# Optimization experiments

Measured on AMD Instinct MI355X. Metric: run time of the kernel, lower is better.

## Reference

```python
import jax, jax.numpy as jnp
import numpy as np

B, S1, S2 = 8, 2048, 2048
K1_DIM = K2_DIM = 512
PK1_DIM = PK2_DIM = 256
ATT_DIM = 512
DV = 512


def setup_inputs() -> dict:
    key = jax.random.key(0)
    ks = jax.random.split(key, 16)
    s = 0.02
    inp = {
        "k1": jax.random.normal(ks[0], (B, S1, K1_DIM), jnp.float32),
        "k2": jax.random.normal(ks[1], (B, S2, K2_DIM), jnp.float32),
        "preserved_k1": jax.random.normal(ks[2], (B, S1, PK1_DIM), jnp.float32),
        "preserved_k2": jax.random.normal(ks[3], (B, S2, PK2_DIM), jnp.float32),
        "v1": jax.random.normal(ks[4], (B, S1, DV), jnp.float32),
        "v2": jax.random.normal(ks[5], (B, S2, DV), jnp.float32),
        # Linear params stored as [in, out] (x @ W + b == torch Linear)
        "W_k1": jax.random.normal(ks[6], (K1_DIM, ATT_DIM), jnp.float32) * s,
        "b_k1": jnp.zeros((ATT_DIM,), jnp.float32),
        "W_k2": jax.random.normal(ks[7], (K2_DIM, ATT_DIM), jnp.float32) * s,
        "b_k2": jnp.zeros((ATT_DIM,), jnp.float32),
        "W_pk1": jax.random.normal(ks[8], (K1_DIM + PK1_DIM, ATT_DIM), jnp.float32) * s,
        "b_pk1": jnp.zeros((ATT_DIM,), jnp.float32),
        "W_pk2": jax.random.normal(ks[9], (K2_DIM + PK2_DIM, ATT_DIM), jnp.float32) * s,
        "b_pk2": jnp.zeros((ATT_DIM,), jnp.float32),
        # lengths in [S/2, S) so no softmax row is fully masked (original exits on NaN)
        "k1_lengths": jax.random.randint(ks[10], (B,), S1 // 2, S1, jnp.int32).astype(jnp.int64),
        "k2_lengths": jax.random.randint(ks[11], (B,), S2 // 2, S2, jnp.int32).astype(jnp.int64),
    }
    return inp


def _mask(k1_lengths, k2_lengths):
    # Faithful to the original loop: a position is masked iff EXACTLY ONE of
    # (row >= l1) / (col >= l2) holds (mask counter == 1, not >= 1).
    row_over = (jnp.arange(S1)[None, :, None] >= k1_lengths[:, None, None])  # [B,S1,1]
    col_over = (jnp.arange(S2)[None, None, :] >= k2_lengths[:, None, None])  # [B,1,S2]
    return (row_over.astype(jnp.int32) + col_over.astype(jnp.int32)) == 1  # [B,S1,S2]


def reference(k1, k2, preserved_k1, preserved_k2, v1, v2,
              W_k1, b_k1, W_k2, b_k2, W_pk1, b_pk1, W_pk2, b_pk2,
              k1_lengths, k2_lengths):
    pk1 = jnp.concatenate([k1, preserved_k1], axis=-1) @ W_pk1 + b_pk1  # [B,S1,A]
    pk2 = jnp.concatenate([k2, preserved_k2], axis=-1) @ W_pk2 + b_pk2  # [B,S2,A]
    k1p = k1 @ W_k1 + b_k1  # [B,S1,A]
    k2p = k2 @ W_k2 + b_k2  # [B,S2,A]

    score_1 = jnp.einsum("bsa,bta->bst", k1p, pk2)   # [B,S1,S2]
    score_2 = jnp.einsum("bsa,bta->bst", pk1, k2p)   # [B,S1,S2]

    mask = _mask(k1_lengths, k2_lengths)
    score_1 = jnp.where(mask, -jnp.inf, score_1)
    score_2 = jnp.where(mask, -jnp.inf, score_2)

    w1 = jax.nn.softmax(jnp.swapaxes(score_1, 1, 2), axis=-1)  # [B,S2,S1]
    w2 = jax.nn.softmax(score_2, axis=-1)                      # [B,S1,S2]

    o1 = jnp.einsum("bts,bsd->btd", w1, v1)  # [B,S2,DV]
    o2 = jnp.einsum("bst,btd->bsd", w2, v2)  # [B,S1,DV]
    # NOTE: original returns ragged per-sample slices of w1/w2; we return the
    # full padded weight matrices (slice w1[i,:l2,:l1], w2[i,:l1,:l2] to match).
    return (o1, o2, w1, w2)
```

## Files before the change

### kernel.cpp

```cpp
#include <hip/hip_runtime.h>

typedef _Float16 half8 __attribute__((ext_vector_type(8)));
typedef float    floatx4 __attribute__((ext_vector_type(4)));
typedef unsigned short u16;

constexpr int Bn  = 8;
constexpr int Sq  = 2048;
constexpr int KD  = 512;
constexpr int PKD = 256;
constexpr int AD  = 512;
constexpr int DV  = 512;

__device__ __forceinline__ void llds16(const void* g, void* l)
{
    __builtin_amdgcn_global_load_lds(
        (const __attribute__((address_space(1))) unsigned int*)g,
        (__attribute__((address_space(3))) unsigned int*)l, 16, 0, 0);
}

__global__ __launch_bounds__(256)
void transpose_cast_k(const float* __restrict__ in, _Float16* __restrict__ out,
                      int inRows, int inCols, long long bsIn, long long bsOut)
{
    __shared__ float t[32][33];
    const int b = blockIdx.z;
    in  += (long long)b * bsIn;
    out += (long long)b * bsOut;
    const int tx = threadIdx.x & 31;
    const int ty = threadIdx.x >> 5;
    const int c0 = blockIdx.x * 32;
    const int r0 = blockIdx.y * 32;
#pragma unroll
    for (int i = 0; i < 4; ++i)
        t[ty + 8*i][tx] = in[(long long)(r0 + ty + 8*i) * inCols + c0 + tx];
    __syncthreads();
#pragma unroll
    for (int i = 0; i < 4; ++i)
        out[(long long)(c0 + ty + 8*i) * inRows + r0 + tx] = (_Float16)t[tx][ty + 8*i];
}

__global__ __launch_bounds__(256)
void cast_cat_k(const float* __restrict__ x, const float* __restrict__ y,
                _Float16* __restrict__ out)
{
    const int idx = blockIdx.x * 256 + threadIdx.x;
    const int e   = idx * 8;
    const int r   = e / 768;
    const int c   = e % 768;
    const float* src = (c < 512) ? (x + (long long)r * 512 + c)
                                 : (y + (long long)r * 256 + (c - 512));
    const floatx4 f0 = *(const floatx4*)(src);
    const floatx4 f1 = *(const floatx4*)(src + 4);
    half8 h;
#pragma unroll
    for (int j = 0; j < 4; ++j) { h[j] = (_Float16)f0[j]; h[4 + j] = (_Float16)f1[j]; }
    *(half8*)(out + (long long)e) = h;
}

template<bool A_F32, bool OUT_F16>
__global__ __launch_bounds__(256, 2)
void gemm_k(const void* __restrict__ A1v, const void* __restrict__ A2v, int Ksplit,
            int lda1, int lda2, long long bsA,
            const _Float16* __restrict__ Bm, int ldb, long long bsB,
            void* __restrict__ Cv, int ldc, long long bsC,
            const float* __restrict__ bias, int K)
{
    __shared__ __align__(16) unsigned char AsRaw[A_F32 ? 16384 : 8192];
    __shared__ __align__(16) unsigned char BsRaw[8192];

    const int tid  = threadIdx.x;
    const int lane = tid & 63;
    const int wave = tid >> 6;
    const int wm   = (wave >> 1) * 64;
    const int wn   = (wave & 1) * 64;
    const int fr   = lane & 15;
    const int fq   = lane >> 4;

    const int tm = blockIdx.y, tn = blockIdx.x, bz = blockIdx.z;
    const long long aRowBase = (long long)tm * 128;
    const long long bRowBase = (long long)tn * 128;
    const _Float16* Bbase = Bm + (long long)bz * bsB;

    floatx4 acc[4][4];
#pragma unroll
    for (int i = 0; i < 4; ++i)
#pragma unroll
        for (int j = 0; j < 4; ++j) acc[i][j] = (floatx4)0.0f;

    for (int k0 = 0; k0 < K; k0 += 32) {
        __syncthreads();

        if (A_F32) {
            const float* A1 = (const float*)A1v + (long long)bz * bsA;
            const float* A2 = (const float*)A2v;
#pragma unroll
            for (int is = 0; is < 4; ++is) {
                const int r  = (tid >> 3) + is * 32;
                const int ch = (tid & 7) ^ (r & 7);
                const int kk = k0 + ch * 4;
                const float* src = (kk < Ksplit)
                    ? A1 + (aRowBase + r) * lda1 + kk
                    : A2 + (aRowBase + r) * lda2 + (kk - Ksplit);
                llds16(src, AsRaw + tid * 16 + is * 4096);
            }
        } else {
            const _Float16* A1 = (const _Float16*)A1v + (long long)bz * bsA;
#pragma unroll
            for (int is = 0; is < 2; ++is) {
                const int r  = (tid >> 2) + is * 64;
                const int ch = (tid & 3) ^ (r & 3);
                llds16(A1 + (aRowBase + r) * lda1 + k0 + ch * 8,
                       AsRaw + tid * 16 + is * 4096);
            }
        }
#pragma unroll
        for (int is = 0; is < 2; ++is) {
            const int r  = (tid >> 2) + is * 64;
            const int ch = (tid & 3) ^ (r & 3);
            llds16(Bbase + (bRowBase + r) * ldb + k0 + ch * 8,
                   BsRaw + tid * 16 + is * 4096);
        }

        __syncthreads();

        half8 af[4], bf[4];
        if (A_F32) {
            const float* As32 = (const float*)AsRaw;
#pragma unroll
            for (int i = 0; i < 4; ++i) {
                const int r  = wm + i * 16 + fr;
                const int c0 = ((2 * fq) ^ (r & 7)) * 4;
                const int c1 = ((2 * fq + 1) ^ (r & 7)) * 4;
                floatx4 f0 = *(const floatx4*)(As32 + r * 32 + c0);
                floatx4 f1 = *(const floatx4*)(As32 + r * 32 + c1);
                half8 h;
#pragma unroll
                for (int j = 0; j < 4; ++j) {
                    h[j]     = (_Float16)f0[j];
                    h[4 + j] = (_Float16)f1[j];
                }
                af[i] = h;
            }
        } else {
            const _Float16* As16 = (const _Float16*)AsRaw;
#pragma unroll
            for (int i = 0; i < 4; ++i) {
                const int r  = wm + i * 16 + fr;
                const int ch = fq ^ (r & 3);
                af[i] = *(const half8*)(As16 + r * 32 + ch * 8);
            }
        }
        {
            const _Float16* Bs16 = (const _Float16*)BsRaw;
#pragma unroll
            for (int j = 0; j < 4; ++j) {
                const int r  = wn + j * 16 + fr;
                const int ch = fq ^ (r & 3);
                bf[j] = *(const half8*)(Bs16 + r * 32 + ch * 8);
            }
        }
#pragma unroll
        for (int i = 0; i < 4; ++i)
#pragma unroll
            for (int j = 0; j < 4; ++j)
                acc[i][j] = __builtin_amdgcn_mfma_f32_16x16x32_f16(af[i], bf[j], acc[i][j], 0, 0, 0);
    }

    const int crow0 = tm * 128 + wm + fq * 4;
    const int ccol0 = tn * 128 + wn + fr;
    if (OUT_F16) {
        _Float16* C = (_Float16*)Cv + (long long)bz * bsC;
#pragma unroll
        for (int i = 0; i < 4; ++i)
#pragma unroll
            for (int j = 0; j < 4; ++j) {
                const int col = ccol0 + j * 16;
                const float bv = bias[col];
#pragma unroll
                for (int r = 0; r < 4; ++r)
                    C[(long long)(crow0 + i*16 + r) * ldc + col] = (_Float16)(acc[i][j][r] + bv);
            }
    } else {
        float* C = (float*)Cv + (long long)bz * bsC;
#pragma unroll
        for (int i = 0; i < 4; ++i)
#pragma unroll
            for (int j = 0; j < 4; ++j) {
                const int col = ccol0 + j * 16;
#pragma unroll
                for (int r = 0; r < 4; ++r)
                    C[(long long)(crow0 + i*16 + r) * ldc + col] = acc[i][j][r];
            }
    }
}

__global__ __launch_bounds__(512, 2)
void gemm256_k(const _Float16* __restrict__ Am, long long bsA, int lda,
               const _Float16* __restrict__ Bm, long long bsB, int ldb,
               float* __restrict__ Cm, long long bsC, int ldc, int K)
{
    __shared__ __align__(16) _Float16 lds[65536];

    const int lin0 = (blockIdx.z * 8 + blockIdx.y) * 8 + blockIdx.x;
    const int lin  = (lin0 & 7) * 64 + (lin0 >> 3);
    const int tn   = lin & 7;
    const int tm   = (lin >> 3) & 7;
    const int bz   = lin >> 6;

    const int tid  = threadIdx.x;
    const int lane = tid & 63;
    const int wave = tid >> 6;
    const int wm   = (wave >> 2) * 128;
    const int wn   = (wave & 3) * 64;
    const int fr   = lane & 15;
    const int fq   = lane >> 4;

    const _Float16* Ab = Am + (long long)bz * bsA + (long long)tm * 256 * lda;
    const _Float16* Bb = Bm + (long long)bz * bsB + (long long)tn * 256 * ldb;

    const int sr = lane >> 3;
    const int ch = (lane & 7) ^ sr;
    const _Float16* srcA[2][2];
    const _Float16* srcB[2][2];
#pragma unroll
    for (int h = 0; h < 2; ++h)
#pragma unroll
        for (int l = 0; l < 2; ++l) {
            const int r = h * 128 + (wave * 2 + l) * 8 + sr;
            srcA[h][l] = Ab + (long long)r * lda + ch * 8;
            srcB[h][l] = Bb + (long long)r * ldb + ch * 8;
        }

    auto stageA = [&](int kt, int buf) {
#pragma unroll
        for (int h = 0; h < 2; ++h)
#pragma unroll
            for (int l = 0; l < 2; ++l)
                llds16(srcA[h][l] + kt * 64,
                       lds + buf * 32768 + h * 8192 + (wave * 2 + l) * 512 + lane * 8);
    };
    auto stageB = [&](int kt, int buf) {
#pragma unroll
        for (int h = 0; h < 2; ++h)
#pragma unroll
            for (int l = 0; l < 2; ++l)
                llds16(srcB[h][l] + kt * 64,
                       lds + buf * 32768 + 16384 + h * 8192 + (wave * 2 + l) * 512 + lane * 8);
    };

    auto rdA = [&](int buf, int im, int kk) -> half8 {
        const int row = wm + im * 16 + fr;
        const int c   = (kk * 4 + fq) ^ (row & 7);
        return *(const half8*)(lds + buf * 32768 + row * 64 + c * 8);
    };
    auto rdB = [&](int buf, int jn, int kk) -> half8 {
        const int row = wn + jn * 16 + fr;
        const int c   = (kk * 4 + fq) ^ (row & 7);
        return *(const half8*)(lds + buf * 32768 + 16384 + row * 64 + c * 8);
    };

    floatx4 acc[8][4];
#pragma unroll
    for (int i = 0; i < 8; ++i)
#pragma unroll
        for (int j = 0; j < 4; ++j) acc[i][j] = (floatx4)0.0f;

    const int KT = K >> 6;

    stageA(0, 0);
    stageB(0, 0);
    __syncthreads();

    for (int kt = 0; kt < KT; ++kt) {
        const int buf = kt & 1;
        half8 af[4][2], bf[2][2];
#pragma unroll
        for (int q = 0; q < 4; ++q) {
            const int nh = q >> 1;
            const int mh = (q == 1 || q == 2) ? 1 : 0;
            if (q == 0 || q == 2) {
#pragma unroll
                for (int j = 0; j < 2; ++j)
#pragma unroll
                    for (int kk = 0; kk < 2; ++kk)
                        bf[j][kk] = rdB(buf, nh * 2 + j, kk);
            }
            if (q != 2) {
#pragma unroll
                for (int i = 0; i < 4; ++i)
#pragma unroll
                    for (int kk = 0; kk < 2; ++kk)
                        af[i][kk] = rdA(buf, mh * 4 + i, kk);
            }
            if (kt + 1 < KT) {
                if (q == 0)      stageA(kt + 1, buf ^ 1);
                else if (q == 1) stageB(kt + 1, buf ^ 1);
            }
            __builtin_amdgcn_s_barrier();
            __builtin_amdgcn_s_setprio(1);
#pragma unroll
            for (int i = 0; i < 4; ++i)
#pragma unroll
                for (int j = 0; j < 2; ++j)
#pragma unroll
                    for (int kk = 0; kk < 2; ++kk)
                        acc[mh * 4 + i][nh * 2 + j] =
                            __builtin_amdgcn_mfma_f32_16x16x32_f16(
                                af[i][kk], bf[j][kk], acc[mh * 4 + i][nh * 2 + j], 0, 0, 0);
            __builtin_amdgcn_s_setprio(0);
            if (q < 3) __builtin_amdgcn_s_barrier();
        }
        __syncthreads();
    }

    float* Cb = Cm + (long long)bz * bsC;
    const int crow0 = tm * 256 + wm + fq * 4;
    const int ccol0 = tn * 256 + wn + fr;
#pragma unroll
    for (int i = 0; i < 8; ++i)
#pragma unroll
        for (int j = 0; j < 4; ++j) {
            const long long base = (long long)(crow0 + i * 16) * ldc + ccol0 + j * 16;
#pragma unroll
            for (int r = 0; r < 4; ++r)
                Cb[base + (long long)r * ldc] = acc[i][j][r];
        }
}

template<bool OUT_F16>
__global__ __launch_bounds__(512, 2)
void gemm256x128_k(const _Float16* __restrict__ A0, const _Float16* __restrict__ A1,
                   long long bsA, int lda,
                   const _Float16* __restrict__ B0, const _Float16* __restrict__ B1,
                   long long bsB, int ldb,
                   void* __restrict__ C0, void* __restrict__ C1,
                   long long bsC, int ldc,
                   const float* __restrict__ bias0, const float* __restrict__ bias1,
                   int K, int zsplit)
{
    __shared__ __align__(16) _Float16 lds[49152];

    const int gx   = gridDim.x, gy = gridDim.y;
    const int nwg  = gx * gy * gridDim.z;
    const int lin0 = (blockIdx.z * gy + blockIdx.y) * gx + blockIdx.x;
    const int cpx  = nwg >> 3;
    const int lin  = (lin0 & 7) * cpx + (lin0 >> 3);
    const int tn   = lin % gx;
    const int tmp2 = lin / gx;
    const int tm   = tmp2 % gy;
    const int bz   = tmp2 / gy;

    const bool sel = (bz >= zsplit);
    const int  bzl = sel ? (bz - zsplit) : bz;
    const _Float16* Am = sel ? A1 : A0;
    const _Float16* Bm = sel ? B1 : B0;

    const int tid  = threadIdx.x;
    const int lane = tid & 63;
    const int wave = tid >> 6;
    const int wm   = (wave >> 2) * 128;
    const int wn   = (wave & 3) * 32;
    const int fr   = lane & 15;
    const int fq   = lane >> 4;

    const _Float16* Ab = Am + (long long)bzl * bsA + (long long)tm * 256 * lda;
    const _Float16* Bb = Bm + (long long)bzl * bsB + (long long)tn * 128 * ldb;

    const int sr = lane >> 3;
    const int ch = (lane & 7) ^ sr;
    const _Float16* srcA[2][2];
    const _Float16* srcB[2];
#pragma unroll
    for (int h = 0; h < 2; ++h)
#pragma unroll
        for (int l = 0; l < 2; ++l)
            srcA[h][l] = Ab + (long long)(h * 128 + (wave * 2 + l) * 8 + sr) * lda + ch * 8;
#pragma unroll
    for (int l = 0; l < 2; ++l)
        srcB[l] = Bb + (long long)((wave * 2 + l) * 8 + sr) * ldb + ch * 8;

    auto stageA = [&](int kt, int buf) {
#pragma unroll
        for (int h = 0; h < 2; ++h)
#pragma unroll
            for (int l = 0; l < 2; ++l)
                llds16(srcA[h][l] + kt * 64,
                       lds + buf * 24576 + h * 8192 + (wave * 2 + l) * 512 + lane * 8);
    };
    auto stageB = [&](int kt, int buf) {
#pragma unroll
        for (int l = 0; l < 2; ++l)
            llds16(srcB[l] + kt * 64,
                   lds + buf * 24576 + 16384 + (wave * 2 + l) * 512 + lane * 8);
    };

    auto rdA = [&](int buf, int im, int kk) -> half8 {
        const int row = wm + im * 16 + fr;
        const int c   = (kk * 4 + fq) ^ (row & 7);
        return *(const half8*)(lds + buf * 24576 + row * 64 + c * 8);
    };
    auto rdB = [&](int buf, int jn, int kk) -> half8 {
        const int row = wn + jn * 16 + fr;
        const int c   = (kk * 4 + fq) ^ (row & 7);
        return *(const half8*)(lds + buf * 24576 + 16384 + row * 64 + c * 8);
    };

    floatx4 acc[8][2];
#pragma unroll
    for (int i = 0; i < 8; ++i)
#pragma unroll
        for (int j = 0; j < 2; ++j) acc[i][j] = (floatx4)0.0f;

    const int KT = K >> 6;

    stageA(0, 0);
    stageB(0, 0);
    __syncthreads();

    for (int kt = 0; kt < KT; ++kt) {
        const int buf = kt & 1;
        half8 afA[4][2], afB[4][2], bf0[2], bf1[2];

#pragma unroll
        for (int kk = 0; kk < 2; ++kk) bf0[kk] = rdB(buf, 0, kk);
#pragma unroll
        for (int i = 0; i < 4; ++i)
#pragma unroll
            for (int kk = 0; kk < 2; ++kk) afA[i][kk] = rdA(buf, i, kk);
        if (kt + 1 < KT) stageA(kt + 1, buf ^ 1);
        __builtin_amdgcn_s_barrier();
        __builtin_amdgcn_s_setprio(1);
#pragma unroll
        for (int i = 0; i < 4; ++i)
#pragma unroll
            for (int kk = 0; kk < 2; ++kk)
                acc[i][0] = __builtin_amdgcn_mfma_f32_16x16x32_f16(afA[i][kk], bf0[kk], acc[i][0], 0, 0, 0);
        __builtin_amdgcn_s_setprio(0);
        __builtin_amdgcn_s_barrier();

#pragma unroll
        for (int i = 0; i < 4; ++i)
#pragma unroll
            for (int kk = 0; kk < 2; ++kk) afB[i][kk] = rdA(buf, 4 + i, kk);
        if (kt + 1 < KT) stageB(kt + 1, buf ^ 1);
        __builtin_amdgcn_s_barrier();
        __builtin_amdgcn_s_setprio(1);
#pragma unroll
        for (int i = 0; i < 4; ++i)
#pragma unroll
            for (int kk = 0; kk < 2; ++kk)
                acc[4 + i][0] = __builtin_amdgcn_mfma_f32_16x16x32_f16(afB[i][kk], bf0[kk], acc[4 + i][0], 0, 0, 0);
        __builtin_amdgcn_s_setprio(0);
        __builtin_amdgcn_s_barrier();

#pragma unroll
        for (int kk = 0; kk < 2; ++kk) bf1[kk] = rdB(buf, 1, kk);
        __builtin_amdgcn_s_barrier();
        __builtin_amdgcn_s_setprio(1);
#pragma unroll
        for (int i = 0; i < 4; ++i)
#pragma unroll
            for (int kk = 0; kk < 2; ++kk)
                acc[4 + i][1] = __builtin_amdgcn_mfma_f32_16x16x32_f16(afB[i][kk], bf1[kk], acc[4 + i][1], 0, 0, 0);
        __builtin_amdgcn_s_setprio(0);
        __builtin_amdgcn_s_barrier();

        __builtin_amdgcn_s_setprio(1);
#pragma unroll
        for (int i = 0; i < 4; ++i)
#pragma unroll
            for (int kk = 0; kk < 2; ++kk)
                acc[i][1] = __builtin_amdgcn_mfma_f32_16x16x32_f16(afA[i][kk], bf1[kk], acc[i][1], 0, 0, 0);
        __builtin_amdgcn_s_setprio(0);

        __syncthreads();
    }

    const int crow0 = tm * 256 + wm + fq * 4;
    const int ccol0 = tn * 128 + wn + fr;
    if (OUT_F16) {
        const float* bias = sel ? bias1 : bias0;
        _Float16* C = (_Float16*)(sel ? C1 : C0) + (long long)bzl * bsC;
#pragma unroll
        for (int i = 0; i < 8; ++i)
#pragma unroll
            for (int j = 0; j < 2; ++j) {
                const int col = ccol0 + j * 16;
                const float bv = bias[col];
#pragma unroll
                for (int r = 0; r < 4; ++r)
                    C[(long long)(crow0 + i * 16 + r) * ldc + col] = (_Float16)(acc[i][j][r] + bv);
            }
    } else {
        float* C = (float*)(sel ? C1 : C0) + (long long)bzl * bsC;
#pragma unroll
        for (int i = 0; i < 8; ++i)
#pragma unroll
            for (int j = 0; j < 2; ++j) {
                const int col = ccol0 + j * 16;
#pragma unroll
                for (int r = 0; r < 4; ++r)
                    C[(long long)(crow0 + i * 16 + r) * ldc + col] = acc[i][j][r];
            }
    }
}

__device__ __forceinline__ int load_len(const int* __restrict__ p, int b)
{
    return (p[1] == 0) ? p[2 * b] : p[b];
}

__global__ __launch_bounds__(256)
void softmax_mask_k(float* __restrict__ w, _Float16* __restrict__ wh,
                    const int* __restrict__ lenR, const int* __restrict__ lenC)
{
    const int b = blockIdx.y;
    const int r = blockIdx.x;
    const long long rowOff = ((long long)b * Sq + r) * (long long)Sq;
    float* row = w + rowOff;
    const int lr = load_len(lenR, b);
    const int lc = load_len(lenC, b);
    const bool rover = (r >= lr);
    const int tid  = threadIdx.x;
    const int lane = tid & 63;
    const int wave = tid >> 6;

    floatx4 x0 = *(const floatx4*)(row + tid * 8);
    floatx4 x1 = *(const floatx4*)(row + tid * 8 + 4);
    float v[8];
#pragma unroll
    for (int j = 0; j < 4; ++j) { v[j] = x0[j]; v[4 + j] = x1[j]; }

    float m = -3.0e38f;
#pragma unroll
    for (int j = 0; j < 8; ++j) {
        const int c = tid * 8 + j;
        if (rover != (c >= lc)) v[j] = -__builtin_inff();
        m = fmaxf(m, v[j]);
    }
#pragma unroll
    for (int off = 32; off > 0; off >>= 1) m = fmaxf(m, __shfl_xor(m, off, 64));
    __shared__ float redm[4], reds[4];
    if (lane == 0) redm[wave] = m;
    __syncthreads();
    m = fmaxf(fmaxf(redm[0], redm[1]), fmaxf(redm[2], redm[3]));

    float s = 0.f;
#pragma unroll
    for (int j = 0; j < 8; ++j) { v[j] = __expf(v[j] - m); s += v[j]; }
#pragma unroll
    for (int off = 32; off > 0; off >>= 1) s += __shfl_xor(s, off, 64);
    if (lane == 0) reds[wave] = s;
    __syncthreads();
    s = reds[0] + reds[1] + reds[2] + reds[3];
    const float inv = 1.0f / s;
#pragma unroll
    for (int j = 0; j < 4; ++j) { x0[j] = v[j] * inv; x1[j] = v[4 + j] * inv; }
    *(floatx4*)(row + tid * 8)     = x0;
    *(floatx4*)(row + tid * 8 + 4) = x1;
    if (wh != nullptr) {
        half8 h;
#pragma unroll
        for (int j = 0; j < 4; ++j) { h[j] = (_Float16)x0[j]; h[4 + j] = (_Float16)x1[j]; }
        *(half8*)(wh + rowOff + tid * 8) = h;
    }
}

extern "C" void kernel_launch(void* const* d_in, const int* in_sizes, int n_in,
                              void* d_out, int out_size, void* d_ws, size_t ws_size,
                              hipStream_t stream)
{
    (void)in_sizes; (void)n_in; (void)out_size;
    const float* k1    = (const float*)d_in[0];
    const float* k2    = (const float*)d_in[1];
    const float* pk1in = (const float*)d_in[2];
    const float* pk2in = (const float*)d_in[3];
    const float* v1    = (const float*)d_in[4];
    const float* v2    = (const float*)d_in[5];
    const float* W_k1  = (const float*)d_in[6];
    const float* b_k1  = (const float*)d_in[7];
    const float* W_k2  = (const float*)d_in[8];
    const float* b_k2  = (const float*)d_in[9];
    const float* W_pk1 = (const float*)d_in[10];
    const float* b_pk1 = (const float*)d_in[11];
    const float* W_pk2 = (const float*)d_in[12];
    const float* b_pk2 = (const float*)d_in[13];
    const int* len1 = (const int*)d_in[14];
    const int* len2 = (const int*)d_in[15];

    float* out = (float*)d_out;
    float* o1 = out;
    float* o2 = o1 + (long long)Bn * Sq * DV;
    float* w1 = o2 + (long long)Bn * Sq * DV;
    float* w2 = w1 + (long long)Bn * Sq * Sq;

    _Float16* k1p = (_Float16*)o1;
    _Float16* k2p = k1p + (long long)Bn * Sq * AD;
    _Float16* pk1 = (_Float16*)o2;
    _Float16* pk2 = pk1 + (long long)Bn * Sq * AD;
    _Float16* cat1 = pk2 + (long long)Bn * Sq * AD;
    _Float16* cat2 = cat1 + (long long)Bn * Sq * (KD + PKD);

    _Float16* vT1   = (_Float16*)d_ws;
    _Float16* vT2   = vT1 + (long long)Bn * DV * Sq;
    _Float16* WTk1  = vT2 + (long long)Bn * DV * Sq;
    _Float16* WTk2  = WTk1 + AD * KD;
    _Float16* WTpk1 = WTk2 + AD * KD;
    _Float16* WTpk2 = WTpk1 + AD * (KD + PKD);

    const unsigned long long fixedHalves =
        2ull * Bn * DV * Sq + 2ull * AD * KD + 2ull * AD * (KD + PKD);
    _Float16* w1h = (_Float16*)d_ws + fixedHalves;
    _Float16* w2h = w1h + (long long)Bn * Sq * Sq;
    const bool fast =
        ws_size >= (fixedHalves + 2ull * Bn * Sq * Sq) * sizeof(_Float16);

    transpose_cast_k<<<dim3(AD/32, KD/32, 1), 256, 0, stream>>>(W_k1, WTk1, KD, AD, 0, 0);
    transpose_cast_k<<<dim3(AD/32, KD/32, 1), 256, 0, stream>>>(W_k2, WTk2, KD, AD, 0, 0);
    transpose_cast_k<<<dim3(AD/32, (KD+PKD)/32, 1), 256, 0, stream>>>(W_pk1, WTpk1, KD+PKD, AD, 0, 0);
    transpose_cast_k<<<dim3(AD/32, (KD+PKD)/32, 1), 256, 0, stream>>>(W_pk2, WTpk2, KD+PKD, AD, 0, 0);
    transpose_cast_k<<<dim3(DV/32, Sq/32, Bn), 256, 0, stream>>>(v1, vT1, Sq, DV,
        (long long)Sq*DV, (long long)Sq*DV);
    transpose_cast_k<<<dim3(DV/32, Sq/32, Bn), 256, 0, stream>>>(v2, vT2, Sq, DV,
        (long long)Sq*DV, (long long)Sq*DV);
    cast_cat_k<<<dim3((Bn*Sq*(KD+PKD))/(256*8), 1, 1), 256, 0, stream>>>(k1, pk1in, cat1);
    cast_cat_k<<<dim3((Bn*Sq*(KD+PKD))/(256*8), 1, 1), 256, 0, stream>>>(k2, pk2in, cat2);

    gemm256x128_k<true><<<dim3(AD/128, (Bn*Sq)/256, 2), 512, 0, stream>>>(
        cat1, cat2, 0, KD+PKD,
        WTk1, WTk2, 0, KD,
        k1p, k2p, 0, AD,
        b_k1, b_k2, KD, 1);
    gemm256x128_k<true><<<dim3(AD/128, (Bn*Sq)/256, 2), 512, 0, stream>>>(
        cat1, cat2, 0, KD+PKD,
        WTpk1, WTpk2, 0, KD+PKD,
        pk1, pk2, 0, AD,
        b_pk1, b_pk2, KD+PKD, 1);

    const dim3 gScore(Sq/256, Sq/256, Bn);
    gemm256_k<<<gScore, 512, 0, stream>>>(
        pk2, (long long)Sq*AD, AD,
        k1p, (long long)Sq*AD, AD,
        w1, (long long)Sq*Sq, Sq, AD);
    gemm256_k<<<gScore, 512, 0, stream>>>(
        pk1, (long long)Sq*AD, AD,
        k2p, (long long)Sq*AD, AD,
        w2, (long long)Sq*Sq, Sq, AD);

    softmax_mask_k<<<dim3(Sq, Bn), 256, 0, stream>>>(w1, fast ? w1h : nullptr, len2, len1);
    softmax_mask_k<<<dim3(Sq, Bn), 256, 0, stream>>>(w2, fast ? w2h : nullptr, len1, len2);

    if (fast) {
        gemm256x128_k<false><<<dim3(DV/128, Sq/256, 2*Bn), 512, 0, stream>>>(
            w1h, w2h, (long long)Sq*Sq, Sq,
            vT1, vT2, (long long)DV*Sq, Sq,
            o1, o2, (long long)Sq*DV, DV,
            nullptr, nullptr, Sq, Bn);
    } else {
        const dim3 gOut(DV/128, Sq/128, Bn);
        gemm_k<true, false><<<gOut, 256, 0, stream>>>(
            w1, w1, Sq, Sq, Sq, (long long)Sq*Sq,
            vT1, Sq, (long long)DV*Sq,
            o1, DV, (long long)Sq*DV, nullptr, Sq);
        gemm_k<true, false><<<gOut, 256, 0, stream>>>(
            w2, w2, Sq, Sq, Sq, (long long)Sq*Sq,
            vT2, Sq, (long long)DV*Sq,
            o2, DV, (long long)Sq*DV, nullptr, Sq);
    }
}
```

Baseline: 854.1 us.

## Merge launches and write score matrices as fp16 before softmax

```diff
diff --git a/kernel.cpp b/kernel.cpp
--- a/kernel.cpp
+++ b/kernel.cpp
@@ -19,13 +19,17 @@
 }
 
 __global__ __launch_bounds__(256)
-void transpose_cast_k(const float* __restrict__ in, _Float16* __restrict__ out,
-                      int inRows, int inCols, long long bsIn, long long bsOut)
+void transpose_cast_k(const float* __restrict__ in0, const float* __restrict__ in1,
+                      _Float16* __restrict__ out0, _Float16* __restrict__ out1,
+                      int inRows, int inCols, long long bsIn, long long bsOut,
+                      int zsplit)
 {
     __shared__ float t[32][33];
-    const int b = blockIdx.z;
-    in  += (long long)b * bsIn;
-    out += (long long)b * bsOut;
+    const int bz = blockIdx.z;
+    const bool sel = (bz >= zsplit);
+    const int b = sel ? bz - zsplit : bz;
+    const float* in = (sel ? in1 : in0) + (long long)b * bsIn;
+    _Float16* out = (sel ? out1 : out0) + (long long)b * bsOut;
     const int tx = threadIdx.x & 31;
     const int ty = threadIdx.x >> 5;
     const int c0 = blockIdx.x * 32;
@@ -40,9 +44,42 @@
 }
 
 __global__ __launch_bounds__(256)
-void cast_cat_k(const float* __restrict__ x, const float* __restrict__ y,
-                _Float16* __restrict__ out)
-{
+void wT_all_k(const float* __restrict__ Wk1, const float* __restrict__ Wk2,
+              const float* __restrict__ Wpk1, const float* __restrict__ Wpk2,
+              _Float16* __restrict__ Tk1, _Float16* __restrict__ Tk2,
+              _Float16* __restrict__ Tpk1, _Float16* __restrict__ Tpk2)
+{
+    const int z = blockIdx.z;
+    const float* W; _Float16* T; int Krows;
+    if      (z == 0) { W = Wk1;  T = Tk1;  Krows = KD; }
+    else if (z == 1) { W = Wk2;  T = Tk2;  Krows = KD; }
+    else if (z == 2) { W = Wpk1; T = Tpk1; Krows = KD + PKD; }
+    else             { W = Wpk2; T = Tpk2; Krows = KD + PKD; }
+    const int r0 = blockIdx.y * 32;
+    if (r0 >= Krows) return;
+    const int c0 = blockIdx.x * 32;
+    __shared__ float t[32][33];
+    const int tx = threadIdx.x & 31;
+    const int ty = threadIdx.x >> 5;
+#pragma unroll
+    for (int i = 0; i < 4; ++i)
+        t[ty + 8*i][tx] = W[(long long)(r0 + ty + 8*i) * AD + c0 + tx];
+    __syncthreads();
+#pragma unroll
+    for (int i = 0; i < 4; ++i)
+        T[(long long)(c0 + ty + 8*i) * Krows + r0 + tx] = (_Float16)t[tx][ty + 8*i];
+}
+
+__global__ __launch_bounds__(256)
+void cast_cat_k(const float* __restrict__ x0, const float* __restrict__ y0,
+                _Float16* __restrict__ o0,
+                const float* __restrict__ x1, const float* __restrict__ y1,
+                _Float16* __restrict__ o1)
+{
+    const bool sel = (blockIdx.z != 0);
+    const float* x = sel ? x1 : x0;
+    const float* y = sel ? y1 : y0;
+    _Float16* out = sel ? o1 : o0;
     const int idx = blockIdx.x * 256 + threadIdx.x;
     const int e   = idx * 8;
     const int r   = e / 768;
@@ -194,18 +231,28 @@
     }
 }
 
+template<bool OUT16>
 __global__ __launch_bounds__(512, 2)
-void gemm256_k(const _Float16* __restrict__ Am, long long bsA, int lda,
-               const _Float16* __restrict__ Bm, long long bsB, int ldb,
-               float* __restrict__ Cm, long long bsC, int ldc, int K)
+void gemm256_k(const _Float16* __restrict__ A0, const _Float16* __restrict__ A1,
+               const _Float16* __restrict__ B0, const _Float16* __restrict__ B1,
+               void* __restrict__ C0v, void* __restrict__ C1v,
+               long long bsA, int lda, long long bsB, int ldb,
+               long long bsC, int ldc, int K, int zsplit)
 {
     __shared__ __align__(16) _Float16 lds[65536];
 
+    const int nwg  = 64 * gridDim.z;
     const int lin0 = (blockIdx.z * 8 + blockIdx.y) * 8 + blockIdx.x;
-    const int lin  = (lin0 & 7) * 64 + (lin0 >> 3);
+    const int cpx  = nwg >> 3;
+    const int lin  = (lin0 & 7) * cpx + (lin0 >> 3);
     const int tn   = lin & 7;
     const int tm   = (lin >> 3) & 7;
     const int bz   = lin >> 6;
+
+    const bool sel = (bz >= zsplit);
+    const int  bzl = sel ? (bz - zsplit) : bz;
+    const _Float16* Am = sel ? A1 : A0;
+    const _Float16* Bm = sel ? B1 : B0;
 
     const int tid  = threadIdx.x;
     const int lane = tid & 63;
@@ -215,8 +262,8 @@
     const int fr   = lane & 15;
     const int fq   = lane >> 4;
 
-    const _Float16* Ab = Am + (long long)bz * bsA + (long long)tm * 256 * lda;
-    const _Float16* Bb = Bm + (long long)bz * bsB + (long long)tn * 256 * ldb;
+    const _Float16* Ab = Am + (long long)bzl * bsA + (long long)tm * 256 * lda;
+    const _Float16* Bb = Bm + (long long)bzl * bsB + (long long)tn * 256 * ldb;
 
     const int sr = lane >> 3;
     const int ch = (lane & 7) ^ sr;
@@ -313,18 +360,31 @@
         __syncthreads();
     }
 
-    float* Cb = Cm + (long long)bz * bsC;
     const int crow0 = tm * 256 + wm + fq * 4;
     const int ccol0 = tn * 256 + wn + fr;
-#pragma unroll
-    for (int i = 0; i < 8; ++i)
-#pragma unroll
-        for (int j = 0; j < 4; ++j) {
-            const long long base = (long long)(crow0 + i * 16) * ldc + ccol0 + j * 16;
-#pragma unroll
-            for (int r = 0; r < 4; ++r)
-                Cb[base + (long long)r * ldc] = acc[i][j][r];
-        }
+    if (OUT16) {
+        _Float16* Cb = (_Float16*)(sel ? C1v : C0v) + (long long)bzl * bsC;
+#pragma unroll
+        for (int i = 0; i < 8; ++i)
+#pragma unroll
+            for (int j = 0; j < 4; ++j) {
+                const long long base = (long long)(crow0 + i * 16) * ldc + ccol0 + j * 16;
+#pragma unroll
+                for (int r = 0; r < 4; ++r)
+                    Cb[base + (long long)r * ldc] = (_Float16)acc[i][j][r];
+            }
+    } else {
+        float* Cb = (float*)(sel ? C1v : C0v) + (long long)bzl * bsC;
+#pragma unroll
+        for (int i = 0; i < 8; ++i)
+#pragma unroll
+            for (int j = 0; j < 4; ++j) {
+                const long long base = (long long)(crow0 + i * 16) * ldc + ccol0 + j * 16;
+#pragma unroll
+                for (int r = 0; r < 4; ++r)
+                    Cb[base + (long long)r * ldc] = acc[i][j][r];
+            }
+    }
 }
 
 template<bool OUT_F16>
@@ -505,15 +565,188 @@
     }
 }
 
+__global__ __launch_bounds__(512, 2)
+void gemm_proj_k(const _Float16* __restrict__ Acat1, const _Float16* __restrict__ Acat2,
+                 const _Float16* __restrict__ B0, const _Float16* __restrict__ B1,
+                 const _Float16* __restrict__ B2, const _Float16* __restrict__ B3,
+                 _Float16* __restrict__ C0, _Float16* __restrict__ C1,
+                 _Float16* __restrict__ C2, _Float16* __restrict__ C3,
+                 const float* __restrict__ bias0, const float* __restrict__ bias1,
+                 const float* __restrict__ bias2, const float* __restrict__ bias3,
+                 int K0, int K1)
+{
+    __shared__ __align__(16) _Float16 lds[49152];
+
+    const int nwg  = 4 * 64 * 4;
+    const int lin0 = (blockIdx.z * 64 + blockIdx.y) * 4 + blockIdx.x;
+    const int cpx  = nwg >> 3;
+    const int lin  = (lin0 & 7) * cpx + (lin0 >> 3);
+    const int tn   = lin & 3;
+    const int tm   = (lin >> 2) & 63;
+    const int pz   = lin >> 8;
+
+    const _Float16* Am = (pz & 1) ? Acat2 : Acat1;
+    const _Float16* Bm; _Float16* Cm; const float* bias; int K;
+    if      (pz == 0) { Bm = B0; Cm = C0; bias = bias0; K = K0; }
+    else if (pz == 1) { Bm = B1; Cm = C1; bias = bias1; K = K0; }
+    else if (pz == 2) { Bm = B2; Cm = C2; bias = bias2; K = K1; }
+    else              { Bm = B3; Cm = C3; bias = bias3; K = K1; }
+    const int lda = KD + PKD;
+    const int ldb = K;
+    const int ldc = AD;
+
+    const int tid  = threadIdx.x;
+    const int lane = tid & 63;
+    const int wave = tid >> 6;
+    const int wm   = (wave >> 2) * 128;
+    const int wn   = (wave & 3) * 32;
+    const int fr   = lane & 15;
+    const int fq   = lane >> 4;
+
+    const _Float16* Ab = Am + (long long)tm * 256 * lda;
+    const _Float16* Bb = Bm + (long long)tn * 128 * ldb;
+
+    const int sr = lane >> 3;
+    const int ch = (lane & 7) ^ sr;
+    const _Float16* srcA[2][2];
+    const _Float16* srcB[2];
+#pragma unroll
+    for (int h = 0; h < 2; ++h)
+#pragma unroll
+        for (int l = 0; l < 2; ++l)
+            srcA[h][l] = Ab + (long long)(h * 128 + (wave * 2 + l) * 8 + sr) * lda + ch * 8;
+#pragma unroll
+    for (int l = 0; l < 2; ++l)
+        srcB[l] = Bb + (long long)((wave * 2 + l) * 8 + sr) * ldb + ch * 8;
+
+    auto stageA = [&](int kt, int buf) {
+#pragma unroll
+        for (int h = 0; h < 2; ++h)
+#pragma unroll
+            for (int l = 0; l < 2; ++l)
+                llds16(srcA[h][l] + kt * 64,
+                       lds + buf * 24576 + h * 8192 + (wave * 2 + l) * 512 + lane * 8);
+    };
+    auto stageB = [&](int kt, int buf) {
+#pragma unroll
+        for (int l = 0; l < 2; ++l)
+            llds16(srcB[l] + kt * 64,
+                   lds + buf * 24576 + 16384 + (wave * 2 + l) * 512 + lane * 8);
+    };
+
+    auto rdA = [&](int buf, int im, int kk) -> half8 {
+        const int row = wm + im * 16 + fr;
+        const int c   = (kk * 4 + fq) ^ (row & 7);
+        return *(const half8*)(lds + buf * 24576 + row * 64 + c * 8);
+    };
+    auto rdB = [&](int buf, int jn, int kk) -> half8 {
+        const int row = wn + jn * 16 + fr;
+        const int c   = (kk * 4 + fq) ^ (row & 7);
+        return *(const half8*)(lds + buf * 24576 + 16384 + row * 64 + c * 8);
+    };
+
+    floatx4 acc[8][2];
+#pragma unroll
+    for (int i = 0; i < 8; ++i)
+#pragma unroll
+        for (int j = 0; j < 2; ++j) acc[i][j] = (floatx4)0.0f;
+
+    const int KT = K >> 6;
+
+    stageA(0, 0);
+    stageB(0, 0);
+    __syncthreads();
+
+    for (int kt = 0; kt < KT; ++kt) {
+        const int buf = kt & 1;
+        half8 afA[4][2], afB[4][2], bf0[2], bf1[2];
+
+#pragma unroll
+        for (int kk = 0; kk < 2; ++kk) bf0[kk] = rdB(buf, 0, kk);
+#pragma unroll
+        for (int i = 0; i < 4; ++i)
+#pragma unroll
+            for (int kk = 0; kk < 2; ++kk) afA[i][kk] = rdA(buf, i, kk);
+        if (kt + 1 < KT) stageA(kt + 1, buf ^ 1);
+        __builtin_amdgcn_s_barrier();
+        __builtin_amdgcn_s_setprio(1);
+#pragma unroll
+        for (int i = 0; i < 4; ++i)
+#pragma unroll
+            for (int kk = 0; kk < 2; ++kk)
+                acc[i][0] = __builtin_amdgcn_mfma_f32_16x16x32_f16(afA[i][kk], bf0[kk], acc[i][0], 0, 0, 0);
+        __builtin_amdgcn_s_setprio(0);
+        __builtin_amdgcn_s_barrier();
+
+#pragma unroll
+        for (int i = 0; i < 4; ++i)
+#pragma unroll
+            for (int kk = 0; kk < 2; ++kk) afB[i][kk] = rdA(buf, 4 + i, kk);
+        if (kt + 1 < KT) stageB(kt + 1, buf ^ 1);
+        __builtin_amdgcn_s_barrier();
+        __builtin_amdgcn_s_setprio(1);
+#pragma unroll
+        for (int i = 0; i < 4; ++i)
+#pragma unroll
+            for (int kk = 0; kk < 2; ++kk)
+                acc[4 + i][0] = __builtin_amdgcn_mfma_f32_16x16x32_f16(afB[i][kk], bf0[kk], acc[4 + i][0], 0, 0, 0);
+        __builtin_amdgcn_s_setprio(0);
+        __builtin_amdgcn_s_barrier();
+
+#pragma unroll
+        for (int kk = 0; kk < 2; ++kk) bf1[kk] = rdB(buf, 1, kk);
+        __builtin_amdgcn_s_barrier();
+        __builtin_amdgcn_s_setprio(1);
+#pragma unroll
+        for (int i = 0; i < 4; ++i)
+#pragma unroll
+            for (int kk = 0; kk < 2; ++kk)
+                acc[4 + i][1] = __builtin_amdgcn_mfma_f32_16x16x32_f16(afB[i][kk], bf1[kk], acc[4 + i][1], 0, 0, 0);
+        __builtin_amdgcn_s_setprio(0);
+        __builtin_amdgcn_s_barrier();
+
+        __builtin_amdgcn_s_setprio(1);
+#pragma unroll
+        for (int i = 0; i < 4; ++i)
+#pragma unroll
+            for (int kk = 0; kk < 2; ++kk)
+                acc[i][1] = __builtin_amdgcn_mfma_f32_16x16x32_f16(afA[i][kk], bf1[kk], acc[i][1], 0, 0, 0);
+        __builtin_amdgcn_s_setprio(0);
+
+        __syncthreads();
+    }
+
+    const int crow0 = tm * 256 + wm + fq * 4;
+    const int ccol0 = tn * 128 + wn + fr;
+#pragma unroll
+    for (int i = 0; i < 8; ++i)
+#pragma unroll
+        for (int j = 0; j < 2; ++j) {
+            const int col = ccol0 + j * 16;
+            const float bv = bias[col];
+#pragma unroll
+            for (int r = 0; r < 4; ++r)
+                Cm[(long long)(crow0 + i * 16 + r) * ldc + col] = (_Float16)(acc[i][j][r] + bv);
+        }
+}
+
 __device__ __forceinline__ int load_len(const int* __restrict__ p, int b)
 {
     return (p[1] == 0) ? p[2 * b] : p[b];
 }
 
+template<bool F16IN>
 __global__ __launch_bounds__(256)
-void softmax_mask_k(float* __restrict__ w, _Float16* __restrict__ wh,
-                    const int* __restrict__ lenR, const int* __restrict__ lenC)
-{
+void softmax_mask_k(float* __restrict__ w1p, float* __restrict__ w2p,
+                    _Float16* __restrict__ wh1, _Float16* __restrict__ wh2,
+                    const int* __restrict__ len1, const int* __restrict__ len2)
+{
+    const int z = blockIdx.z;
+    float* w = z ? w2p : w1p;
+    _Float16* wh = z ? wh2 : wh1;
+    const int* lenR = z ? len1 : len2;
+    const int* lenC = z ? len2 : len1;
+
     const int b = blockIdx.y;
     const int r = blockIdx.x;
     const long long rowOff = ((long long)b * Sq + r) * (long long)Sq;
@@ -525,11 +758,17 @@
     const int lane = tid & 63;
     const int wave = tid >> 6;
 
-    floatx4 x0 = *(const floatx4*)(row + tid * 8);
-    floatx4 x1 = *(const floatx4*)(row + tid * 8 + 4);
     float v[8];
-#pragma unroll
-    for (int j = 0; j < 4; ++j) { v[j] = x0[j]; v[4 + j] = x1[j]; }
+    if (F16IN) {
+        const half8 hv = *(const half8*)(wh + rowOff + tid * 8);
+#pragma unroll
+        for (int j = 0; j < 8; ++j) v[j] = (float)hv[j];
+    } else {
+        const floatx4 x0 = *(const floatx4*)(row + tid * 8);
+        const floatx4 x1 = *(const floatx4*)(row + tid * 8 + 4);
+#pragma unroll
+        for (int j = 0; j < 4; ++j) { v[j] = x0[j]; v[4 + j] = x1[j]; }
+    }
 
     float m = -3.0e38f;
 #pragma unroll
@@ -554,11 +793,13 @@
     __syncthreads();
     s = reds[0] + reds[1] + reds[2] + reds[3];
     const float inv = 1.0f / s;
+
+    floatx4 x0, x1;
 #pragma unroll
     for (int j = 0; j < 4; ++j) { x0[j] = v[j] * inv; x1[j] = v[4 + j] * inv; }
     *(floatx4*)(row + tid * 8)     = x0;
     *(floatx4*)(row + tid * 8 + 4) = x1;
-    if (wh != nullptr) {
+    if (F16IN || wh != nullptr) {
         half8 h;
 #pragma unroll
         for (int j = 0; j < 4; ++j) { h[j] = (_Float16)x0[j]; h[4 + j] = (_Float16)x1[j]; }
@@ -615,40 +856,39 @@
     const bool fast =
         ws_size >= (fixedHalves + 2ull * Bn * Sq * Sq) * sizeof(_Float16);
 
-    transpose_cast_k<<<dim3(AD/32, KD/32, 1), 256, 0, stream>>>(W_k1, WTk1, KD, AD, 0, 0);
-    transpose_cast_k<<<dim3(AD/32, KD/32, 1), 256, 0, stream>>>(W_k2, WTk2, KD, AD, 0, 0);
-    transpose_cast_k<<<dim3(AD/32, (KD+PKD)/32, 1), 256, 0, stream>>>(W_pk1, WTpk1, KD+PKD, AD, 0, 0);
-    transpose_cast_k<<<dim3(AD/32, (KD+PKD)/32, 1), 256, 0, stream>>>(W_pk2, WTpk2, KD+PKD, AD, 0, 0);
-    transpose_cast_k<<<dim3(DV/32, Sq/32, Bn), 256, 0, stream>>>(v1, vT1, Sq, DV,
-        (long long)Sq*DV, (long long)Sq*DV);
-    transpose_cast_k<<<dim3(DV/32, Sq/32, Bn), 256, 0, stream>>>(v2, vT2, Sq, DV,
-        (long long)Sq*DV, (long long)Sq*DV);
-    cast_cat_k<<<dim3((Bn*Sq*(KD+PKD))/(256*8), 1, 1), 256, 0, stream>>>(k1, pk1in, cat1);
-    cast_cat_k<<<dim3((Bn*Sq*(KD+PKD))/(256*8), 1, 1), 256, 0, stream>>>(k2, pk2in, cat2);
-
-    gemm256x128_k<true><<<dim3(AD/128, (Bn*Sq)/256, 2), 512, 0, stream>>>(
-        cat1, cat2, 0, KD+PKD,
-        WTk1, WTk2, 0, KD,
-        k1p, k2p, 0, AD,
-        b_k1, b_k2, KD, 1);
-    gemm256x128_k<true><<<dim3(AD/128, (Bn*Sq)/256, 2), 512, 0, stream>>>(
-        cat1, cat2, 0, KD+PKD,
-        WTpk1, WTpk2, 0, KD+PKD,
-        pk1, pk2, 0, AD,
-        b_pk1, b_pk2, KD+PKD, 1);
-
-    const dim3 gScore(Sq/256, Sq/256, Bn);
-    gemm256_k<<<gScore, 512, 0, stream>>>(
-        pk2, (long long)Sq*AD, AD,
-        k1p, (long long)Sq*AD, AD,
-        w1, (long long)Sq*Sq, Sq, AD);
-    gemm256_k<<<gScore, 512, 0, stream>>>(
-        pk1, (long long)Sq*AD, AD,
-        k2p, (long long)Sq*AD, AD,
-        w2, (long long)Sq*Sq, Sq, AD);
-
-    softmax_mask_k<<<dim3(Sq, Bn), 256, 0, stream>>>(w1, fast ? w1h : nullptr, len2, len1);
-    softmax_mask_k<<<dim3(Sq, Bn), 256, 0, stream>>>(w2, fast ? w2h : nullptr, len1, len2);
+    wT_all_k<<<dim3(AD/32, (KD+PKD)/32, 4), 256, 0, stream>>>(
+        W_k1, W_k2, W_pk1, W_pk2, WTk1, WTk2, WTpk1, WTpk2);
+    transpose_cast_k<<<dim3(DV/32, Sq/32, 2*Bn), 256, 0, stream>>>(
+        v1, v2, vT1, vT2, Sq, DV, (long long)Sq*DV, (long long)Sq*DV, Bn);
+    cast_cat_k<<<dim3((Bn*Sq*(KD+PKD))/(256*8), 1, 2), 256, 0, stream>>>(
+        k1, pk1in, cat1, k2, pk2in, cat2);
+
+    gemm_proj_k<<<dim3(AD/128, (Bn*Sq)/256, 4), 512, 0, stream>>>(
+        cat1, cat2,
+        WTk1, WTk2, WTpk1, WTpk2,
+        k1p, k2p, pk1, pk2,
+        b_k1, b_k2, b_pk1, b_pk2,
+        KD, KD + PKD);
+
+    if (fast) {
+        gemm256_k<true><<<dim3(Sq/256, Sq/256, 2*Bn), 512, 0, stream>>>(
+            pk2, pk1, k1p, k2p, w1h, w2h,
+            (long long)Sq*AD, AD, (long long)Sq*AD, AD,
+            (long long)Sq*Sq, Sq, AD, Bn);
+    } else {
+        gemm256_k<false><<<dim3(Sq/256, Sq/256, 2*Bn), 512, 0, stream>>>(
+            pk2, pk1, k1p, k2p, w1, w2,
+            (long long)Sq*AD, AD, (long long)Sq*AD, AD,
+            (long long)Sq*Sq, Sq, AD, Bn);
+    }
+
+    if (fast) {
+        softmax_mask_k<true><<<dim3(Sq, Bn, 2), 256, 0, stream>>>(
+            w1, w2, w1h, w2h, len1, len2);
+    } else {
+        softmax_mask_k<false><<<dim3(Sq, Bn, 2), 256, 0, stream>>>(
+            w1, w2, nullptr, nullptr, len1, len2);
+    }
 
     if (fast) {
         gemm256x128_k<false><<<dim3(DV/128, Sq/256, 2*Bn), 512, 0, stream>>>(
```

Result: faster. 792.1 us (-7.3%).
